# Kernel optimization log

Measured on AMD Instinct MI355X. Metric: run time of the kernel, lower is better.

Reference implementation:

```python
import jax, jax.numpy as jnp
import numpy as np

C, W, H = 256, 64, 192
RECORD_LEN = np.array([5, 3, 4, 2, 5, 3, 4, 2], dtype=np.int64)  # sums to 28


def setup_inputs() -> dict:
    key = jax.random.key(0)
    total = int(RECORD_LEN.sum())
    x = jax.random.normal(key, (total, C, W, H), dtype=jnp.float32)
    record_len = jnp.asarray(RECORD_LEN)
    return {"x": x, "record_len": record_len}


def _group_attention(xx):
    # xx: [L, C, W, H] -> per-pixel self-attention over the L agents, d_model = C
    L = xx.shape[0]
    q = xx.reshape(L, C, W * H).transpose(2, 0, 1)          # [N=W*H, L, C]
    score = jnp.einsum('nlc,nmc->nlm', q, q) / jnp.sqrt(jnp.float32(C))
    attn = jax.nn.softmax(score, axis=-1)                    # [N, L, L]
    # original keeps only ego agent (row 0) of the context
    ctx0 = jnp.einsum('nm,nmc->nc', attn[:, 0, :], q)        # [N, C]
    out = ctx0.T.reshape(1, C, W, H)
    attn_maps = attn.transpose(1, 2, 0).reshape(L, L, W, H)
    return out, attn_maps


def reference(x, record_len):
    rl = np.asarray(record_len)  # static ragged lengths
    offsets = np.concatenate([[0], np.cumsum(rl)])
    outs = []
    attn_last = None
    for i in range(len(rl)):  # small fixed number of ragged groups
        xx = x[int(offsets[i]):int(offsets[i + 1])]
        out_i, attn_last = _group_attention(xx)
        outs.append(out_i)
    # matches torch: returns fused ego features per scene + attn of LAST group
    return jnp.concatenate(outs, axis=0), attn_last
```

## Files before the change

kernel.cpp:

```cpp
#include <hip/hip_runtime.h>
#include <hip/hip_bf16.h>
#include <math.h>

#define C_DIM 256
#define W_DIM 64
#define H_DIM 192
#define WH (W_DIM * H_DIM)
#define NGROUPS 8
#define BLOCKS_PER_GROUP (WH / 256)

template <int L, bool WRITE_ATTN>
__device__ __forceinline__ void att_group_body(
    const float* __restrict__ xg,
    float* __restrict__ out,
    float* __restrict__ attn_out,
    int n)
{
    constexpr int NTRI = L * (L + 1) / 2;
    float s[NTRI];
#pragma unroll
    for (int i = 0; i < NTRI; ++i) s[i] = 0.0f;

#pragma unroll 4
    for (int c = 0; c < C_DIM; ++c) {
        float v[L];
#pragma unroll
        for (int l = 0; l < L; ++l)
            v[l] = xg[(l * C_DIM + c) * WH + n];
        int idx = 0;
#pragma unroll
        for (int l = 0; l < L; ++l)
#pragma unroll
            for (int m = l; m < L; ++m)
                s[idx++] += v[l] * v[m];
    }

    const float scale = 0.0625f;

    float p0[L];
    float mx = -INFINITY;
#pragma unroll
    for (int m = 0; m < L; ++m) {
        p0[m] = s[m] * scale;
        mx = fmaxf(mx, p0[m]);
    }
    float sum = 0.0f;
#pragma unroll
    for (int m = 0; m < L; ++m) {
        p0[m] = __expf(p0[m] - mx);
        sum += p0[m];
    }
    const float inv = 1.0f / sum;
#pragma unroll
    for (int m = 0; m < L; ++m) p0[m] *= inv;

    if constexpr (WRITE_ATTN) {
        float g[L][L];
        int idx = 0;
#pragma unroll
        for (int l = 0; l < L; ++l)
#pragma unroll
            for (int m = l; m < L; ++m) {
                const float v = s[idx++] * scale;
                g[l][m] = v;
                g[m][l] = v;
            }
#pragma unroll
        for (int l = 0; l < L; ++l) {
            float mx2 = -INFINITY;
#pragma unroll
            for (int m = 0; m < L; ++m) mx2 = fmaxf(mx2, g[l][m]);
            float e[L];
            float sm = 0.0f;
#pragma unroll
            for (int m = 0; m < L; ++m) {
                e[m] = __expf(g[l][m] - mx2);
                sm += e[m];
            }
            const float iv = 1.0f / sm;
#pragma unroll
            for (int m = 0; m < L; ++m)
                attn_out[(l * L + m) * WH + n] = e[m] * iv;
        }
    }

#pragma unroll 4
    for (int c = 0; c < C_DIM; ++c) {
        float acc = 0.0f;
#pragma unroll
        for (int m = 0; m < L; ++m)
            acc += p0[m] * xg[(m * C_DIM + c) * WH + n];
        out[c * WH + n] = acc;
    }
}

__global__ __launch_bounds__(256) void att_fused_kernel(
    const float* __restrict__ x,
    float* __restrict__ out0,
    float* __restrict__ attn)
{
    const int b = blockIdx.x;
    const int g = b / BLOCKS_PER_GROUP;
    const int bn = b - g * BLOCKS_PER_GROUP;
    const int n = bn * 256 + threadIdx.x;

    const int offs[NGROUPS] = {0, 5, 8, 12, 14, 19, 22, 26};
    const int lens[NGROUPS] = {5, 3, 4, 2, 5, 3, 4, 2};

    const float* xg = x + (size_t)offs[g] * C_DIM * WH;
    float* og = out0 + (size_t)g * C_DIM * WH;

    switch (lens[g]) {
        case 5: att_group_body<5, false>(xg, og, nullptr, n); break;
        case 4: att_group_body<4, false>(xg, og, nullptr, n); break;
        case 3: att_group_body<3, false>(xg, og, nullptr, n); break;
        case 2:
            if (g == NGROUPS - 1)
                att_group_body<2, true>(xg, og, attn, n);
            else
                att_group_body<2, false>(xg, og, nullptr, n);
            break;
    }
}

extern "C" void kernel_launch(void* const* d_in, const int* in_sizes, int n_in,
                              void* d_out, int out_size, void* d_ws, size_t ws_size,
                              hipStream_t stream) {
    const float* x = (const float*)d_in[0];
    float* out0 = (float*)d_out;
    float* attn = out0 + (size_t)NGROUPS * C_DIM * WH;

    const dim3 grid(NGROUPS * BLOCKS_PER_GROUP);
    const dim3 block(256);
    att_fused_kernel<<<grid, block, 0, stream>>>(x, out0, attn);
}
```

Before: 564.9 us.

## Split Gram and context into two kernels with channel-chunked parallelism

Splits the fused kernel into a Gram kernel that computes partial upper-triangle dot products over four channel chunks into workspace, and a context kernel that sums those partials, applies the softmax and writes the output for its channel chunk. This gives four times as many blocks to raise occupancy and latency hiding. The context kernel runs groups in reverse order, possibly to reuse recently cached x, and uses nontemporal loads and stores. The cost is a second full read of x, extra workspace traffic and a second launch.

```diff
diff --git a/kernel.cpp b/kernel.cpp
--- a/kernel.cpp
+++ b/kernel.cpp
@@ -1,5 +1,4 @@
 #include <hip/hip_runtime.h>
-#include <hip/hip_bf16.h>
 #include <math.h>
 
 #define C_DIM 256
@@ -7,32 +6,87 @@
 #define H_DIM 192
 #define WH (W_DIM * H_DIM)
 #define NGROUPS 8
-#define BLOCKS_PER_GROUP (WH / 256)
+#define NCHUNK 4
+#define CCHUNK (C_DIM / NCHUNK)
+#define NBLK (WH / 256)
+#define TRI_TOTAL 68
+
+template <int L>
+__device__ __forceinline__ void gram_partial_body(
+    const float* __restrict__ xg,
+    float* __restrict__ wsg,
+    const int c0, const int n)
+{
+    constexpr int NTRI = L * (L + 1) / 2;
+    float s[NTRI];
+#pragma unroll
+    for (int i = 0; i < NTRI; ++i) s[i] = 0.0f;
+
+#pragma unroll 4
+    for (int cc = 0; cc < CCHUNK; ++cc) {
+        const int c = c0 + cc;
+        float v[L];
+#pragma unroll
+        for (int l = 0; l < L; ++l)
+            v[l] = xg[(size_t)(l * C_DIM + c) * WH + n];
+        int idx = 0;
+#pragma unroll
+        for (int l = 0; l < L; ++l)
+#pragma unroll
+            for (int m = l; m < L; ++m)
+                s[idx++] += v[l] * v[m];
+    }
+
+#pragma unroll
+    for (int i = 0; i < NTRI; ++i)
+        wsg[(size_t)i * WH + n] = s[i];
+}
+
+__global__ __launch_bounds__(256) void gram_kernel(
+    const float* __restrict__ x,
+    float* __restrict__ ws)
+{
+    const int b = blockIdx.x;
+    const int g = b / (NCHUNK * NBLK);
+    const int rem = b - g * (NCHUNK * NBLK);
+    const int chunk = rem / NBLK;
+    const int bn = rem - chunk * NBLK;
+    const int n = bn * 256 + threadIdx.x;
+    const int c0 = chunk * CCHUNK;
+
+    const int offs[NGROUPS]    = {0, 5, 8, 12, 14, 19, 22, 26};
+    const int lens[NGROUPS]    = {5, 3, 4, 2, 5, 3, 4, 2};
+    const int triBase[NGROUPS] = {0, 15, 21, 31, 34, 49, 55, 65};
+
+    const float* xg = x + (size_t)offs[g] * C_DIM * WH;
+    float* wsg = ws + (size_t)(chunk * TRI_TOTAL + triBase[g]) * WH;
+
+    switch (lens[g]) {
+        case 5: gram_partial_body<5>(xg, wsg, c0, n); break;
+        case 4: gram_partial_body<4>(xg, wsg, c0, n); break;
+        case 3: gram_partial_body<3>(xg, wsg, c0, n); break;
+        case 2: gram_partial_body<2>(xg, wsg, c0, n); break;
+    }
+}
 
 template <int L, bool WRITE_ATTN>
-__device__ __forceinline__ void att_group_body(
+__device__ __forceinline__ void ctx_body(
     const float* __restrict__ xg,
+    const float* __restrict__ wsg,
     float* __restrict__ out,
     float* __restrict__ attn_out,
-    int n)
+    const int c0, const int n)
 {
     constexpr int NTRI = L * (L + 1) / 2;
+
     float s[NTRI];
 #pragma unroll
-    for (int i = 0; i < NTRI; ++i) s[i] = 0.0f;
-
-#pragma unroll 4
-    for (int c = 0; c < C_DIM; ++c) {
-        float v[L];
-#pragma unroll
-        for (int l = 0; l < L; ++l)
-            v[l] = xg[(l * C_DIM + c) * WH + n];
-        int idx = 0;
-#pragma unroll
-        for (int l = 0; l < L; ++l)
-#pragma unroll
-            for (int m = l; m < L; ++m)
-                s[idx++] += v[l] * v[m];
+    for (int i = 0; i < NTRI; ++i) {
+        float acc = 0.0f;
+#pragma unroll
+        for (int ch = 0; ch < NCHUNK; ++ch)
+            acc += wsg[(size_t)(ch * TRI_TOTAL + i) * WH + n];
+        s[i] = acc;
     }
 
     const float scale = 0.0625f;
@@ -55,70 +109,79 @@
     for (int m = 0; m < L; ++m) p0[m] *= inv;
 
     if constexpr (WRITE_ATTN) {
-        float g[L][L];
+        float gm[L][L];
         int idx = 0;
 #pragma unroll
         for (int l = 0; l < L; ++l)
 #pragma unroll
             for (int m = l; m < L; ++m) {
                 const float v = s[idx++] * scale;
-                g[l][m] = v;
-                g[m][l] = v;
+                gm[l][m] = v;
+                gm[m][l] = v;
             }
 #pragma unroll
         for (int l = 0; l < L; ++l) {
             float mx2 = -INFINITY;
 #pragma unroll
-            for (int m = 0; m < L; ++m) mx2 = fmaxf(mx2, g[l][m]);
+            for (int m = 0; m < L; ++m) mx2 = fmaxf(mx2, gm[l][m]);
             float e[L];
             float sm = 0.0f;
 #pragma unroll
             for (int m = 0; m < L; ++m) {
-                e[m] = __expf(g[l][m] - mx2);
+                e[m] = __expf(gm[l][m] - mx2);
                 sm += e[m];
             }
             const float iv = 1.0f / sm;
 #pragma unroll
             for (int m = 0; m < L; ++m)
-                attn_out[(l * L + m) * WH + n] = e[m] * iv;
+                attn_out[(size_t)(l * L + m) * WH + n] = e[m] * iv;
         }
     }
 
 #pragma unroll 4
-    for (int c = 0; c < C_DIM; ++c) {
+    for (int cc = 0; cc < CCHUNK; ++cc) {
+        const int c = c0 + cc;
         float acc = 0.0f;
 #pragma unroll
         for (int m = 0; m < L; ++m)
-            acc += p0[m] * xg[(m * C_DIM + c) * WH + n];
-        out[c * WH + n] = acc;
-    }
-}
-
-__global__ __launch_bounds__(256) void att_fused_kernel(
+            acc += p0[m] * __builtin_nontemporal_load(
+                              &xg[(size_t)(m * C_DIM + c) * WH + n]);
+        __builtin_nontemporal_store(acc, &out[(size_t)c * WH + n]);
+    }
+}
+
+__global__ __launch_bounds__(256) void ctx_kernel(
     const float* __restrict__ x,
+    const float* __restrict__ ws,
     float* __restrict__ out0,
     float* __restrict__ attn)
 {
     const int b = blockIdx.x;
-    const int g = b / BLOCKS_PER_GROUP;
-    const int bn = b - g * BLOCKS_PER_GROUP;
+    const int gi = b / (NCHUNK * NBLK);
+    const int g = NGROUPS - 1 - gi;
+    const int rem = b - gi * (NCHUNK * NBLK);
+    const int chunk = rem / NBLK;
+    const int bn = rem - chunk * NBLK;
     const int n = bn * 256 + threadIdx.x;
-
-    const int offs[NGROUPS] = {0, 5, 8, 12, 14, 19, 22, 26};
-    const int lens[NGROUPS] = {5, 3, 4, 2, 5, 3, 4, 2};
+    const int c0 = chunk * CCHUNK;
+
+    const int offs[NGROUPS]    = {0, 5, 8, 12, 14, 19, 22, 26};
+    const int lens[NGROUPS]    = {5, 3, 4, 2, 5, 3, 4, 2};
+    const int triBase[NGROUPS] = {0, 15, 21, 31, 34, 49, 55, 65};
 
     const float* xg = x + (size_t)offs[g] * C_DIM * WH;
+    const float* wsg = ws + (size_t)triBase[g] * WH;
     float* og = out0 + (size_t)g * C_DIM * WH;
 
     switch (lens[g]) {
-        case 5: att_group_body<5, false>(xg, og, nullptr, n); break;
-        case 4: att_group_body<4, false>(xg, og, nullptr, n); break;
-        case 3: att_group_body<3, false>(xg, og, nullptr, n); break;
+        case 5: ctx_body<5, false>(xg, wsg, og, nullptr, c0, n); break;
+        case 4: ctx_body<4, false>(xg, wsg, og, nullptr, c0, n); break;
+        case 3: ctx_body<3, false>(xg, wsg, og, nullptr, c0, n); break;
         case 2:
-            if (g == NGROUPS - 1)
-                att_group_body<2, true>(xg, og, attn, n);
+            if (g == NGROUPS - 1 && chunk == 0)
+                ctx_body<2, true>(xg, wsg, og, attn, c0, n);
             else
-                att_group_body<2, false>(xg, og, nullptr, n);
+                ctx_body<2, false>(xg, wsg, og, nullptr, c0, n);
             break;
     }
 }
@@ -129,8 +192,10 @@
     const float* x = (const float*)d_in[0];
     float* out0 = (float*)d_out;
     float* attn = out0 + (size_t)NGROUPS * C_DIM * WH;
-
-    const dim3 grid(NGROUPS * BLOCKS_PER_GROUP);
+    float* ws = (float*)d_ws;
+
+    const dim3 grid(NGROUPS * NCHUNK * NBLK);
     const dim3 block(256);
-    att_fused_kernel<<<grid, block, 0, stream>>>(x, out0, attn);
-}
+    gram_kernel<<<grid, block, 0, stream>>>(x, ws);
+    ctx_kernel<<<grid, block, 0, stream>>>(x, ws, out0, attn);
+}
```

Result: faster. 541.9 us (-4.1%).

## Split channel reduction across four wavefronts per pixel tile with LDS reduction

Applied to the files above, without the earlier changes.

Each block now covers 64 pixels, with four wavefronts each handling a quarter of the channels. Partial Gram sums are combined through shared memory, so the grid grows fourfold and more waves are in flight to hide memory latency. The second pass over x uses nontemporal loads, and the outputs use nontemporal stores. The cost is an LDS buffer and a block barrier, and each wave's global accesses now cover only 64 contiguous floats per row instead of 256.

```diff
diff --git a/kernel.cpp b/kernel.cpp
--- a/kernel.cpp
+++ b/kernel.cpp
@@ -1,5 +1,4 @@
 #include <hip/hip_runtime.h>
-#include <hip/hip_bf16.h>
 #include <math.h>
 
 #define C_DIM 256
@@ -7,26 +6,34 @@
 #define H_DIM 192
 #define WH (W_DIM * H_DIM)
 #define NGROUPS 8
-#define BLOCKS_PER_GROUP (WH / 256)
+#define NCHUNK 4
+#define CCHUNK (C_DIM / NCHUNK)
+#define NLOC 64
+#define NBLK (WH / NLOC)
+#define MAXTRI 15
 
 template <int L, bool WRITE_ATTN>
-__device__ __forceinline__ void att_group_body(
+__device__ __forceinline__ void att_body(
     const float* __restrict__ xg,
     float* __restrict__ out,
     float* __restrict__ attn_out,
-    int n)
+    float* __restrict__ lds,
+    const int n, const int chunk, const int nl)
 {
     constexpr int NTRI = L * (L + 1) / 2;
+
     float s[NTRI];
 #pragma unroll
     for (int i = 0; i < NTRI; ++i) s[i] = 0.0f;
 
+    const int c0 = chunk * CCHUNK;
 #pragma unroll 4
-    for (int c = 0; c < C_DIM; ++c) {
+    for (int cc = 0; cc < CCHUNK; ++cc) {
+        const int c = c0 + cc;
         float v[L];
 #pragma unroll
         for (int l = 0; l < L; ++l)
-            v[l] = xg[(l * C_DIM + c) * WH + n];
+            v[l] = xg[(size_t)(l * C_DIM + c) * WH + n];
         int idx = 0;
 #pragma unroll
         for (int l = 0; l < L; ++l)
@@ -35,13 +42,28 @@
                 s[idx++] += v[l] * v[m];
     }
 
+#pragma unroll
+    for (int i = 0; i < NTRI; ++i)
+        lds[i * 256 + chunk * NLOC + nl] = s[i];
+    __syncthreads();
+
+    float sf[NTRI];
+#pragma unroll
+    for (int i = 0; i < NTRI; ++i) {
+        float a = lds[i * 256 + nl];
+#pragma unroll
+        for (int ch = 1; ch < NCHUNK; ++ch)
+            a += lds[i * 256 + ch * NLOC + nl];
+        sf[i] = a;
+    }
+
     const float scale = 0.0625f;
 
     float p0[L];
     float mx = -INFINITY;
 #pragma unroll
     for (int m = 0; m < L; ++m) {
-        p0[m] = s[m] * scale;
+        p0[m] = sf[m] * scale;
         mx = fmaxf(mx, p0[m]);
     }
     float sum = 0.0f;
@@ -55,42 +77,47 @@
     for (int m = 0; m < L; ++m) p0[m] *= inv;
 
     if constexpr (WRITE_ATTN) {
-        float g[L][L];
-        int idx = 0;
+        if (chunk == 0) {
+            float gm[L][L];
+            int idx = 0;
 #pragma unroll
-        for (int l = 0; l < L; ++l)
+            for (int l = 0; l < L; ++l)
 #pragma unroll
-            for (int m = l; m < L; ++m) {
-                const float v = s[idx++] * scale;
-                g[l][m] = v;
-                g[m][l] = v;
+                for (int m = l; m < L; ++m) {
+                    const float v = sf[idx++] * scale;
+                    gm[l][m] = v;
+                    gm[m][l] = v;
+                }
+#pragma unroll
+            for (int l = 0; l < L; ++l) {
+                float mx2 = -INFINITY;
+#pragma unroll
+                for (int m = 0; m < L; ++m) mx2 = fmaxf(mx2, gm[l][m]);
+                float e[L];
+                float sm = 0.0f;
+#pragma unroll
+                for (int m = 0; m < L; ++m) {
+                    e[m] = __expf(gm[l][m] - mx2);
+                    sm += e[m];
+                }
+                const float iv = 1.0f / sm;
+#pragma unroll
+                for (int m = 0; m < L; ++m)
+                    __builtin_nontemporal_store(
+                        e[m] * iv, &attn_out[(size_t)(l * L + m) * WH + n]);
             }
-#pragma unroll
-        for (int l = 0; l < L; ++l) {
-            float mx2 = -INFINITY;
-#pragma unroll
-            for (int m = 0; m < L; ++m) mx2 = fmaxf(mx2, g[l][m]);
-            float e[L];
-            float sm = 0.0f;
-#pragma unroll
-            for (int m = 0; m < L; ++m) {
-                e[m] = __expf(g[l][m] - mx2);
-                sm += e[m];
-            }
-            const float iv = 1.0f / sm;
-#pragma unroll
-            for (int m = 0; m < L; ++m)
-                attn_out[(l * L + m) * WH + n] = e[m] * iv;
         }
     }
 
 #pragma unroll 4
-    for (int c = 0; c < C_DIM; ++c) {
+    for (int cc = 0; cc < CCHUNK; ++cc) {
+        const int c = c0 + cc;
         float acc = 0.0f;
 #pragma unroll
         for (int m = 0; m < L; ++m)
-            acc += p0[m] * xg[(m * C_DIM + c) * WH + n];
-        out[c * WH + n] = acc;
+            acc += p0[m] * __builtin_nontemporal_load(
+                              &xg[(size_t)(m * C_DIM + c) * WH + n]);
+        __builtin_nontemporal_store(acc, &out[(size_t)c * WH + n]);
     }
 }
 
@@ -99,10 +126,14 @@
     float* __restrict__ out0,
     float* __restrict__ attn)
 {
+    __shared__ float lds[MAXTRI * 256];
+
     const int b = blockIdx.x;
-    const int g = b / BLOCKS_PER_GROUP;
-    const int bn = b - g * BLOCKS_PER_GROUP;
-    const int n = bn * 256 + threadIdx.x;
+    const int g = b / NBLK;
+    const int bn = b - g * NBLK;
+    const int chunk = threadIdx.x >> 6;
+    const int nl = threadIdx.x & 63;
+    const int n = bn * NLOC + nl;
 
     const int offs[NGROUPS] = {0, 5, 8, 12, 14, 19, 22, 26};
     const int lens[NGROUPS] = {5, 3, 4, 2, 5, 3, 4, 2};
@@ -111,14 +142,14 @@
     float* og = out0 + (size_t)g * C_DIM * WH;
 
     switch (lens[g]) {
-        case 5: att_group_body<5, false>(xg, og, nullptr, n); break;
-        case 4: att_group_body<4, false>(xg, og, nullptr, n); break;
-        case 3: att_group_body<3, false>(xg, og, nullptr, n); break;
+        case 5: att_body<5, false>(xg, og, nullptr, lds, n, chunk, nl); break;
+        case 4: att_body<4, false>(xg, og, nullptr, lds, n, chunk, nl); break;
+        case 3: att_body<3, false>(xg, og, nullptr, lds, n, chunk, nl); break;
         case 2:
             if (g == NGROUPS - 1)
-                att_group_body<2, true>(xg, og, attn, n);
+                att_body<2, true>(xg, og, attn, lds, n, chunk, nl);
             else
-                att_group_body<2, false>(xg, og, nullptr, n);
+                att_body<2, false>(xg, og, nullptr, lds, n, chunk, nl);
             break;
     }
 }
@@ -130,7 +161,7 @@
     float* out0 = (float*)d_out;
     float* attn = out0 + (size_t)NGROUPS * C_DIM * WH;
 
-    const dim3 grid(NGROUPS * BLOCKS_PER_GROUP);
+    const dim3 grid(NGROUPS * NBLK);
     const dim3 block(256);
     att_fused_kernel<<<grid, block, 0, stream>>>(x, out0, attn);
 }
```

New measurement: 532.2 us. 1.06x faster.
